# Performance work log

Hardware: AMD Instinct MI355X
Metric: run time of the kernel (lower is better)

Reference implementation:

```python
import jax, jax.numpy as jnp
import numpy as np

EPS = 1e-12

def setup_inputs() -> dict:
    key = jax.random.key(0)
    k1, k2, k3 = jax.random.split(key, 3)
    B, D, N, NCLS = 1024, 512, 100000, 1000
    z = jax.random.normal(k1, (B, D), dtype=jnp.float32)
    lab_bank = jax.random.normal(k2, (N, D), dtype=jnp.float32)
    lab_labels = jax.random.randint(k3, (N,), 0, NCLS, dtype=jnp.int64)
    return {"z": z, "lab_bank": lab_bank, "lab_labels": lab_labels, "topk": 5}

def reference(z, lab_bank, lab_labels, topk):
    # cosine similarity: normalize query and bank, then GEMM
    zn = z / jnp.maximum(jnp.linalg.norm(z, axis=-1, keepdims=True), EPS)            # [B, D]
    bn = lab_bank / jnp.maximum(jnp.linalg.norm(lab_bank, axis=-1, keepdims=True), EPS)  # [N, D]
    sim = jnp.einsum('bd,nd->bn', zn, bn)                                            # [B, N]
    top_vals, top_idx = jax.lax.top_k(sim, topk)                                     # [B, k] each
    labels = lab_labels[top_idx]                                                     # [B, k]
    return top_idx, top_vals, labels
```

## Files before the change

### kernel.cpp

```cpp
#include <hip/hip_runtime.h>
#include <math.h>

#define DDIM 512
#define NS 96
#define SPITCH 132
#define KMASK 0xFFFFF800
#define NEG_INF (-3.0e38f)
#define IMAX 0x7fffffff

typedef _Float16 f16x8 __attribute__((ext_vector_type(8)));
typedef float    f32x4 __attribute__((ext_vector_type(4)));
typedef int      i32x4 __attribute__((ext_vector_type(4)));

__device__ __forceinline__ int imin(int a, int b) { return a < b ? a : b; }
__device__ __forceinline__ int imax(int a, int b) { return a > b ? a : b; }

__device__ __forceinline__ int med3(int a, int b, int c) {
    int d;
    asm("v_med3_i32 %0, %1, %2, %3" : "=v"(d) : "v"(a), "v"(b), "v"(c));
    return d;
}

__device__ __forceinline__ void glds16(const void* g, void* l) {
    __builtin_amdgcn_global_load_lds((const __attribute__((address_space(1))) void*)g,
                                     (__attribute__((address_space(3))) void*)l, 16, 0, 0);
}

#define KBAR() do { asm volatile("s_waitcnt vmcnt(0)" ::: "memory"); \
                    __builtin_amdgcn_s_barrier();                    \
                    asm volatile("" ::: "memory"); } while (0)
#define EBAR() do { asm volatile("s_waitcnt lgkmcnt(0)" ::: "memory"); \
                    __builtin_amdgcn_s_barrier();                      \
                    asm volatile("" ::: "memory"); } while (0)

__global__ __launch_bounds__(256) void split_tile_k(const float* __restrict__ src,
                                                    unsigned* __restrict__ tile,
                                                    float* __restrict__ rn, int rows) {
    const int t = threadIdx.x;
    const int r = t >> 1, hf = t & 1;
    const int R = blockIdx.x * 128 + r;
    const bool valid = R < rows;
    const float* srow = src + (size_t)(valid ? R : 0) * DDIM + hf * 16;
    float ss = 0.f;
    for (int ks = 0; ks < 16; ++ks) {
        float4 v0 = *(const float4*)(srow + ks * 32);
        float4 v1 = *(const float4*)(srow + ks * 32 + 4);
        float4 v2 = *(const float4*)(srow + ks * 32 + 8);
        float4 v3 = *(const float4*)(srow + ks * 32 + 12);
        ss += v0.x*v0.x + v0.y*v0.y + v0.z*v0.z + v0.w*v0.w
            + v1.x*v1.x + v1.y*v1.y + v1.z*v1.z + v1.w*v1.w
            + v2.x*v2.x + v2.y*v2.y + v2.z*v2.z + v2.w*v2.w
            + v3.x*v3.x + v3.y*v3.y + v3.z*v3.z + v3.w*v3.w;
        unsigned o[8];
        o[0] = __builtin_bit_cast(unsigned, __builtin_amdgcn_cvt_pkrtz(v0.x, v0.y));
        o[1] = __builtin_bit_cast(unsigned, __builtin_amdgcn_cvt_pkrtz(v0.z, v0.w));
        o[2] = __builtin_bit_cast(unsigned, __builtin_amdgcn_cvt_pkrtz(v1.x, v1.y));
        o[3] = __builtin_bit_cast(unsigned, __builtin_amdgcn_cvt_pkrtz(v1.z, v1.w));
        o[4] = __builtin_bit_cast(unsigned, __builtin_amdgcn_cvt_pkrtz(v2.x, v2.y));
        o[5] = __builtin_bit_cast(unsigned, __builtin_amdgcn_cvt_pkrtz(v2.z, v2.w));
        o[6] = __builtin_bit_cast(unsigned, __builtin_amdgcn_cvt_pkrtz(v3.x, v3.y));
        o[7] = __builtin_bit_cast(unsigned, __builtin_amdgcn_cvt_pkrtz(v3.z, v3.w));
        if (!valid) {
            #pragma unroll
            for (int q = 0; q < 8; ++q) o[q] = 0u;
        }
        unsigned* dst = tile + ((size_t)(blockIdx.x * 16 + ks) * 128 + r) * 16 + hf * 8;
        *(i32x4*)dst       = *(i32x4*)o;
        *(i32x4*)(dst + 4) = *(i32x4*)(o + 4);
    }
    ss += __shfl_xor(ss, 1, 64);
    if (hf == 0) rn[R] = valid ? 1.0f / fmaxf(sqrtf(ss), 1e-12f) : 0.0f;
}

__global__ __launch_bounds__(256, 3) void gemm_screen_k(
    const unsigned* __restrict__ zh, const unsigned* __restrict__ bh,
    const float* __restrict__ rb,
    int* __restrict__ cand, int N, int nChunks) {

    __shared__ alignas(16) int smem[12544];
    int* SIMI = smem + 4096;

    const int t = threadIdx.x;
    const int w = t >> 6, lane = t & 63;
    const int wm = w & 1, wn = w >> 1;
    const int quad = lane >> 4, l16 = lane & 15;
    const int split = blockIdx.x, rowblk = blockIdx.y;
    const int soff = w * 1024 + lane * 16;

    int t0 = (int)0x80000000, t1 = t0, t2 = t0, t3 = t0;

    {
        const char* gA = (const char*)zh + (size_t)(rowblk * 16) * 8192;
        const char* gB = (const char*)bh + (size_t)(split * 16) * 8192;
        glds16(gA + soff,        (char*)smem + soff);
        glds16(gA + 4096 + soff, (char*)smem + 4096 + soff);
        glds16(gB + soff,        (char*)smem + 8192 + soff);
        glds16(gB + 4096 + soff, (char*)smem + 12288 + soff);
    }

    int iter = 0;
    for (int chunk = split; chunk < nChunks; chunk += NS, ++iter) {
        f32x4 acc[4][4];
        #pragma unroll
        for (int mi = 0; mi < 4; ++mi)
            #pragma unroll
            for (int ni = 0; ni < 4; ++ni) acc[mi][ni] = (f32x4){0.f, 0.f, 0.f, 0.f};
        float rbv[4];

        #pragma unroll 2
        for (int ks = 0; ks < 16; ++ks) {
            KBAR();
            if (ks < 15) {
                const char* gA = (const char*)zh + (size_t)(rowblk * 16 + ks + 1) * 8192;
                const char* gB = (const char*)bh + (size_t)(chunk * 16 + ks + 1) * 8192;
                char* l = (char*)smem + (((ks & 1) ^ 1) << 14);
                glds16(gA + soff,        l + soff);
                glds16(gA + 4096 + soff, l + 4096 + soff);
                glds16(gB + soff,        l + 8192 + soff);
                glds16(gB + 4096 + soff, l + 12288 + soff);
            } else if (chunk + NS < nChunks) {
                const char* gA = (const char*)zh + (size_t)(rowblk * 16) * 8192;
                const char* gB = (const char*)bh + (size_t)((chunk + NS) * 16) * 8192;
                glds16(gA + soff,        (char*)smem + soff);
                glds16(gA + 4096 + soff, (char*)smem + 4096 + soff);
                glds16(gB + soff,        (char*)smem + 8192 + soff);
                glds16(gB + 4096 + soff, (char*)smem + 12288 + soff);
            }
            if (ks == 0) {
                #pragma unroll
                for (int ni = 0; ni < 4; ++ni)
                    rbv[ni] = rb[chunk * 128 + wn * 64 + ni * 16 + l16];
            }

            const unsigned short* A  = (const unsigned short*)((const char*)smem + ((ks & 1) << 14));
            const unsigned short* Bb = (const unsigned short*)((const char*)smem + ((ks & 1) << 14) + 8192);
            f16x8 af[4], bf[4];
            #pragma unroll
            for (int mi = 0; mi < 4; ++mi)
                af[mi] = __builtin_bit_cast(f16x8,
                    *(const i32x4*)(A + (wm * 64 + mi * 16 + l16) * 32 + quad * 8));
            #pragma unroll
            for (int ni = 0; ni < 4; ++ni)
                bf[ni] = __builtin_bit_cast(f16x8,
                    *(const i32x4*)(Bb + (wn * 64 + ni * 16 + l16) * 32 + quad * 8));
            #pragma unroll
            for (int mi = 0; mi < 4; ++mi)
                #pragma unroll
                for (int ni = 0; ni < 4; ++ni)
                    acc[mi][ni] = __builtin_amdgcn_mfma_f32_16x16x32_f16(af[mi], bf[ni], acc[mi][ni], 0, 0, 0);
        }

        const int iterTag = iter << 7;
        #pragma unroll
        for (int p = 0; p < 2; ++p) {
            EBAR();
            #pragma unroll
            for (int nj = 0; nj < 2; ++nj) {
                const int ni = p * 2 + nj;
                const int cCol = wn * 64 + ni * 16 + l16;
                const int tagc = iterTag | cCol;
                const float rv = rbv[ni];
                const int cp = wn * 32 + nj * 16 + l16;
                #pragma unroll
                for (int mi = 0; mi < 4; ++mi) {
                    i32x4 kv;
                    #pragma unroll
                    for (int rr = 0; rr < 4; ++rr) {
                        float v = acc[mi][ni][rr] * rv;
                        kv[rr] = (__float_as_int(v) & KMASK) | tagc;
                    }
                    *(i32x4*)(SIMI + cp * SPITCH + wm * 64 + mi * 16 + quad * 4) = kv;
                }
            }
            EBAR();
            {
                const int r = t >> 1, h = t & 1;
                const int* s = SIMI + (h * 32) * SPITCH + r;
                #pragma unroll
                for (int j = 0; j < 32; ++j) {
                    int kk = s[j * SPITCH];
                    int n1 = med3(kk, t0, t1);
                    int n2 = med3(kk, t1, t2);
                    int n3 = med3(kk, t2, t3);
                    t0 = imax(kk, t0);
                    t1 = n1; t2 = n2; t3 = n3;
                }
            }
        }
    }

    const int r = t >> 1, h = t & 1;
    i32x4 outk = { t0, t1, t2, t3 };
    *(i32x4*)(cand + (((size_t)(rowblk * 128 + r) * NS + split) * 2 + h) * 4) = outk;
}

__global__ __launch_bounds__(256) void merge_rescore_k(
    const int* __restrict__ cand,
    const float* __restrict__ z, const float* __restrict__ bank,
    const float* __restrict__ rz, const float* __restrict__ rb,
    const int* __restrict__ labels, float* __restrict__ out, int BK, int N) {

    __shared__ float zrow[DDIM];
    __shared__ int   idxs[32];
    __shared__ float dots[32];

    const int row = blockIdx.x;
    const int t = threadIdx.x, w = t >> 6, lane = t & 63;

    {   float2 v = *(const float2*)(z + (size_t)row * DDIM + t * 2);
        zrow[t * 2] = v.x; zrow[t * 2 + 1] = v.y; }

    if (w == 0) {
        int k[12];
        const int* cp = cand + (size_t)row * (NS * 2 * 4) + lane * 12;
        #pragma unroll
        for (int q = 0; q < 12; ++q) k[q] = cp[q];
        for (int r = 0; r < 32; ++r) {
            int lk = k[0], lq = 0;
            #pragma unroll
            for (int q = 1; q < 12; ++q) if (k[q] > lk) { lk = k[q]; lq = q; }
            int wk = lk, wl = lane, wq = lq;
            #pragma unroll
            for (int off = 32; off > 0; off >>= 1) {
                int ok = __shfl_xor(wk, off, 64);
                int ol = __shfl_xor(wl, off, 64);
                int oq = __shfl_xor(wq, off, 64);
                if (ok > wk || (ok == wk && ol < wl)) { wk = ok; wl = ol; wq = oq; }
            }
            if (lane == wl) {
                #pragma unroll
                for (int q = 0; q < 12; ++q) if (q == wq) k[q] = (int)0x80000000;
            }
            if (lane == 0) {
                int j = wl * 12 + wq;
                int split = j >> 3;
                int c = wk & 127, it = (wk >> 7) & 15;
                int gi = (it * NS + split) * 128 + c;
                idxs[r] = gi < N ? gi : 0;
            }
        }
    }
    __syncthreads();

    #pragma unroll
    for (int jj = 0; jj < 8; ++jj) {
        const int ci = idxs[w * 8 + jj];
        const float* br = bank + (size_t)ci * DDIM + lane * 8;
        float4 x0 = *(const float4*)br;
        float4 x1 = *(const float4*)(br + 4);
        const float* zz = zrow + lane * 8;
        float4 z0 = *(const float4*)zz;
        float4 z1 = *(const float4*)(zz + 4);
        float s = x0.x*z0.x + x0.y*z0.y + x0.z*z0.z + x0.w*z0.w
                + x1.x*z1.x + x1.y*z1.y + x1.z*z1.z + x1.w*z1.w;
        #pragma unroll
        for (int off = 32; off > 0; off >>= 1) s += __shfl_xor(s, off, 64);
        if (lane == 0) dots[w * 8 + jj] = s;
    }
    __syncthreads();

    if (w == 0) {
        const float rzv = rz[row];
        float v; int ii;
        if (lane < 32) { ii = idxs[lane]; v = dots[lane] * rzv * rb[ii]; }
        else           { ii = IMAX;       v = NEG_INF; }
        for (int r = 0; r < 5; ++r) {
            float bv = v; int bi = ii;
            #pragma unroll
            for (int off = 32; off > 0; off >>= 1) {
                float ov = __shfl_xor(bv, off, 64);
                int   oi = __shfl_xor(bi, off, 64);
                if (ov > bv || (ov == bv && oi < bi)) { bv = ov; bi = oi; }
            }
            if (v == bv && ii == bi) { v = NEG_INF; ii = IMAX; }
            if (lane == 0) {
                out[(size_t)row * 5 + r]          = (float)bi;
                out[BK + (size_t)row * 5 + r]     = bv;
                out[2 * BK + (size_t)row * 5 + r] = (float)labels[bi];
            }
        }
    }
}

extern "C" void kernel_launch(void* const* d_in, const int* in_sizes, int n_in,
                              void* d_out, int out_size, void* d_ws, size_t ws_size,
                              hipStream_t stream) {
    const float* z    = (const float*)d_in[0];
    const float* bank = (const float*)d_in[1];
    const int*   lab  = (const int*)d_in[2];
    const int B = in_sizes[0] / DDIM;
    const int N = in_sizes[1] / DDIM;
    const int BK = out_size / 3;
    const int nChunks = (N + 127) >> 7;
    float* out = (float*)d_out;
    char* ws = (char*)d_ws;

    const size_t o_rz = 0;
    const size_t o_rb = 4096;
    const size_t o_zh = o_rb + (size_t)nChunks * 128 * 4;
    const size_t o_bh = o_zh + (size_t)(B / 128) * 16 * 8192;
    const size_t o_cv = o_bh + (size_t)nChunks * 16 * 8192;

    float* rz = (float*)(ws + o_rz);
    float* rb = (float*)(ws + o_rb);
    unsigned* zh = (unsigned*)(ws + o_zh);
    unsigned* bh = (unsigned*)(ws + o_bh);
    int* cand = (int*)(ws + o_cv);

    split_tile_k<<<nChunks, 256, 0, stream>>>(bank, bh, rb, N);
    split_tile_k<<<B / 128, 256, 0, stream>>>(z, zh, rz, B);
    gemm_screen_k<<<dim3(NS, B / 128), 256, 0, stream>>>(zh, bh, rb, cand, N, nChunks);
    merge_rescore_k<<<B, 256, 0, stream>>>(cand, z, bank, rz, rb, lab, out, BK, N);
}
```

Baseline: 484.1 us.

## Pre-normalize tiles and do top-4 screening in registers, dropping LDS transpose

The tiling kernel now computes the row norm first and writes already-normalized fp16 tiles, so the GEMM no longer loads or applies bank norms. The GEMM epilogue keeps per-thread top-4 lists in registers straight from the MFMA accumulators, with the operand order swapped so each lane holds consecutive bank columns. These lists are merged across lanes with shuffles at the end, which removes the shared-memory staging and its barriers and frees LDS for higher occupancy (launch bounds 3 -> 4). The two tiling launches are also merged into one. In exchange, the source rows are read twice in the tiling kernel and register pressure rises from 16 top-k slots per thread.

```diff
diff --git a/kernel.cpp b/kernel.cpp
--- a/kernel.cpp
+++ b/kernel.cpp
@@ -3,7 +3,6 @@
 
 #define DDIM 512
 #define NS 96
-#define SPITCH 132
 #define KMASK 0xFFFFF800
 #define NEG_INF (-3.0e38f)
 #define IMAX 0x7fffffff
@@ -29,18 +28,24 @@
 #define KBAR() do { asm volatile("s_waitcnt vmcnt(0)" ::: "memory"); \
                     __builtin_amdgcn_s_barrier();                    \
                     asm volatile("" ::: "memory"); } while (0)
-#define EBAR() do { asm volatile("s_waitcnt lgkmcnt(0)" ::: "memory"); \
-                    __builtin_amdgcn_s_barrier();                      \
-                    asm volatile("" ::: "memory"); } while (0)
-
-__global__ __launch_bounds__(256) void split_tile_k(const float* __restrict__ src,
-                                                    unsigned* __restrict__ tile,
-                                                    float* __restrict__ rn, int rows) {
+
+__global__ __launch_bounds__(256) void split_tile_k(
+    const float* __restrict__ zsrc, const float* __restrict__ bsrc,
+    unsigned* __restrict__ ztile, unsigned* __restrict__ btile,
+    float* __restrict__ rz, float* __restrict__ rb,
+    int zrows, int brows, int nbBlocks) {
+
+    const int bx = blockIdx.x;
+    const float* src; unsigned* tile; float* rn; int rows; int blk;
+    if (bx < nbBlocks) { src = bsrc; tile = btile; rn = rb; rows = brows; blk = bx; }
+    else               { src = zsrc; tile = ztile; rn = rz; rows = zrows; blk = bx - nbBlocks; }
+
     const int t = threadIdx.x;
     const int r = t >> 1, hf = t & 1;
-    const int R = blockIdx.x * 128 + r;
+    const int R = blk * 128 + r;
     const bool valid = R < rows;
     const float* srow = src + (size_t)(valid ? R : 0) * DDIM + hf * 16;
+
     float ss = 0.f;
     for (int ks = 0; ks < 16; ++ks) {
         float4 v0 = *(const float4*)(srow + ks * 32);
@@ -51,43 +56,49 @@
             + v1.x*v1.x + v1.y*v1.y + v1.z*v1.z + v1.w*v1.w
             + v2.x*v2.x + v2.y*v2.y + v2.z*v2.z + v2.w*v2.w
             + v3.x*v3.x + v3.y*v3.y + v3.z*v3.z + v3.w*v3.w;
+    }
+    ss += __shfl_xor(ss, 1, 64);
+    const float scale = valid ? 1.0f / fmaxf(sqrtf(ss), 1e-12f) : 0.0f;
+    if (hf == 0) rn[R] = scale;
+
+    for (int ks = 0; ks < 16; ++ks) {
+        float4 v0 = *(const float4*)(srow + ks * 32);
+        float4 v1 = *(const float4*)(srow + ks * 32 + 4);
+        float4 v2 = *(const float4*)(srow + ks * 32 + 8);
+        float4 v3 = *(const float4*)(srow + ks * 32 + 12);
         unsigned o[8];
-        o[0] = __builtin_bit_cast(unsigned, __builtin_amdgcn_cvt_pkrtz(v0.x, v0.y));
-        o[1] = __builtin_bit_cast(unsigned, __builtin_amdgcn_cvt_pkrtz(v0.z, v0.w));
-        o[2] = __builtin_bit_cast(unsigned, __builtin_amdgcn_cvt_pkrtz(v1.x, v1.y));
-        o[3] = __builtin_bit_cast(unsigned, __builtin_amdgcn_cvt_pkrtz(v1.z, v1.w));
-        o[4] = __builtin_bit_cast(unsigned, __builtin_amdgcn_cvt_pkrtz(v2.x, v2.y));
-        o[5] = __builtin_bit_cast(unsigned, __builtin_amdgcn_cvt_pkrtz(v2.z, v2.w));
-        o[6] = __builtin_bit_cast(unsigned, __builtin_amdgcn_cvt_pkrtz(v3.x, v3.y));
-        o[7] = __builtin_bit_cast(unsigned, __builtin_amdgcn_cvt_pkrtz(v3.z, v3.w));
-        if (!valid) {
-            #pragma unroll
-            for (int q = 0; q < 8; ++q) o[q] = 0u;
-        }
-        unsigned* dst = tile + ((size_t)(blockIdx.x * 16 + ks) * 128 + r) * 16 + hf * 8;
+        o[0] = __builtin_bit_cast(unsigned, __builtin_amdgcn_cvt_pkrtz(v0.x*scale, v0.y*scale));
+        o[1] = __builtin_bit_cast(unsigned, __builtin_amdgcn_cvt_pkrtz(v0.z*scale, v0.w*scale));
+        o[2] = __builtin_bit_cast(unsigned, __builtin_amdgcn_cvt_pkrtz(v1.x*scale, v1.y*scale));
+        o[3] = __builtin_bit_cast(unsigned, __builtin_amdgcn_cvt_pkrtz(v1.z*scale, v1.w*scale));
+        o[4] = __builtin_bit_cast(unsigned, __builtin_amdgcn_cvt_pkrtz(v2.x*scale, v2.y*scale));
+        o[5] = __builtin_bit_cast(unsigned, __builtin_amdgcn_cvt_pkrtz(v2.z*scale, v2.w*scale));
+        o[6] = __builtin_bit_cast(unsigned, __builtin_amdgcn_cvt_pkrtz(v3.x*scale, v3.y*scale));
+        o[7] = __builtin_bit_cast(unsigned, __builtin_amdgcn_cvt_pkrtz(v3.z*scale, v3.w*scale));
+        unsigned* dst = tile + ((size_t)(blk * 16 + ks) * 128 + r) * 16 + hf * 8;
         *(i32x4*)dst       = *(i32x4*)o;
         *(i32x4*)(dst + 4) = *(i32x4*)(o + 4);
     }
-    ss += __shfl_xor(ss, 1, 64);
-    if (hf == 0) rn[R] = valid ? 1.0f / fmaxf(sqrtf(ss), 1e-12f) : 0.0f;
-}
-
-__global__ __launch_bounds__(256, 3) void gemm_screen_k(
+}
+
+__global__ __launch_bounds__(256, 4) void gemm_screen_k(
     const unsigned* __restrict__ zh, const unsigned* __restrict__ bh,
-    const float* __restrict__ rb,
     int* __restrict__ cand, int N, int nChunks) {
 
-    __shared__ alignas(16) int smem[12544];
-    int* SIMI = smem + 4096;
+    __shared__ alignas(16) int smem[8192];
 
     const int t = threadIdx.x;
     const int w = t >> 6, lane = t & 63;
-    const int wm = w & 1, wn = w >> 1;
+    const int wz = w >> 1, wb = w & 1;
     const int quad = lane >> 4, l16 = lane & 15;
     const int split = blockIdx.x, rowblk = blockIdx.y;
     const int soff = w * 1024 + lane * 16;
 
-    int t0 = (int)0x80000000, t1 = t0, t2 = t0, t3 = t0;
+    int T[4][4];
+    #pragma unroll
+    for (int zi = 0; zi < 4; ++zi)
+        #pragma unroll
+        for (int q = 0; q < 4; ++q) T[zi][q] = (int)0x80000000;
 
     {
         const char* gA = (const char*)zh + (size_t)(rowblk * 16) * 8192;
@@ -102,10 +113,9 @@
     for (int chunk = split; chunk < nChunks; chunk += NS, ++iter) {
         f32x4 acc[4][4];
         #pragma unroll
-        for (int mi = 0; mi < 4; ++mi)
-            #pragma unroll
-            for (int ni = 0; ni < 4; ++ni) acc[mi][ni] = (f32x4){0.f, 0.f, 0.f, 0.f};
-        float rbv[4];
+        for (int bi = 0; bi < 4; ++bi)
+            #pragma unroll
+            for (int zi = 0; zi < 4; ++zi) acc[bi][zi] = (f32x4){0.f, 0.f, 0.f, 0.f};
 
         #pragma unroll 2
         for (int ks = 0; ks < 16; ++ks) {
@@ -126,72 +136,60 @@
                 glds16(gB + soff,        (char*)smem + 8192 + soff);
                 glds16(gB + 4096 + soff, (char*)smem + 12288 + soff);
             }
-            if (ks == 0) {
-                #pragma unroll
-                for (int ni = 0; ni < 4; ++ni)
-                    rbv[ni] = rb[chunk * 128 + wn * 64 + ni * 16 + l16];
-            }
 
             const unsigned short* A  = (const unsigned short*)((const char*)smem + ((ks & 1) << 14));
             const unsigned short* Bb = (const unsigned short*)((const char*)smem + ((ks & 1) << 14) + 8192);
             f16x8 af[4], bf[4];
             #pragma unroll
-            for (int mi = 0; mi < 4; ++mi)
-                af[mi] = __builtin_bit_cast(f16x8,
-                    *(const i32x4*)(A + (wm * 64 + mi * 16 + l16) * 32 + quad * 8));
-            #pragma unroll
-            for (int ni = 0; ni < 4; ++ni)
-                bf[ni] = __builtin_bit_cast(f16x8,
-                    *(const i32x4*)(Bb + (wn * 64 + ni * 16 + l16) * 32 + quad * 8));
-            #pragma unroll
-            for (int mi = 0; mi < 4; ++mi)
+            for (int zi = 0; zi < 4; ++zi)
+                af[zi] = __builtin_bit_cast(f16x8,
+                    *(const i32x4*)(A + (wz * 64 + zi * 16 + l16) * 32 + quad * 8));
+            #pragma unroll
+            for (int bi = 0; bi < 4; ++bi)
+                bf[bi] = __builtin_bit_cast(f16x8,
+                    *(const i32x4*)(Bb + (wb * 64 + bi * 16 + l16) * 32 + quad * 8));
+            #pragma unroll
+            for (int bi = 0; bi < 4; ++bi)
                 #pragma unroll
-                for (int ni = 0; ni < 4; ++ni)
-                    acc[mi][ni] = __builtin_amdgcn_mfma_f32_16x16x32_f16(af[mi], bf[ni], acc[mi][ni], 0, 0, 0);
-        }
-
-        const int iterTag = iter << 7;
-        #pragma unroll
-        for (int p = 0; p < 2; ++p) {
-            EBAR();
-            #pragma unroll
-            for (int nj = 0; nj < 2; ++nj) {
-                const int ni = p * 2 + nj;
-                const int cCol = wn * 64 + ni * 16 + l16;
-                const int tagc = iterTag | cCol;
-                const float rv = rbv[ni];
-                const int cp = wn * 32 + nj * 16 + l16;
+                for (int zi = 0; zi < 4; ++zi)
+                    acc[bi][zi] = __builtin_amdgcn_mfma_f32_16x16x32_f16(bf[bi], af[zi], acc[bi][zi], 0, 0, 0);
+        }
+
+        const int tbase = (iter << 7) | (wb << 6) | (quad << 2);
+        #pragma unroll
+        for (int zi = 0; zi < 4; ++zi)
+            #pragma unroll
+            for (int bi = 0; bi < 4; ++bi)
                 #pragma unroll
-                for (int mi = 0; mi < 4; ++mi) {
-                    i32x4 kv;
-                    #pragma unroll
-                    for (int rr = 0; rr < 4; ++rr) {
-                        float v = acc[mi][ni][rr] * rv;
-                        kv[rr] = (__float_as_int(v) & KMASK) | tagc;
-                    }
-                    *(i32x4*)(SIMI + cp * SPITCH + wm * 64 + mi * 16 + quad * 4) = kv;
+                for (int rr = 0; rr < 4; ++rr) {
+                    int kk = (__float_as_int(acc[bi][zi][rr]) & KMASK) | (tbase + bi * 16 + rr);
+                    int n1 = med3(kk, T[zi][0], T[zi][1]);
+                    int n2 = med3(kk, T[zi][1], T[zi][2]);
+                    int n3 = med3(kk, T[zi][2], T[zi][3]);
+                    T[zi][0] = imax(kk, T[zi][0]);
+                    T[zi][1] = n1; T[zi][2] = n2; T[zi][3] = n3;
                 }
-            }
-            EBAR();
-            {
-                const int r = t >> 1, h = t & 1;
-                const int* s = SIMI + (h * 32) * SPITCH + r;
-                #pragma unroll
-                for (int j = 0; j < 32; ++j) {
-                    int kk = s[j * SPITCH];
-                    int n1 = med3(kk, t0, t1);
-                    int n2 = med3(kk, t1, t2);
-                    int n3 = med3(kk, t2, t3);
-                    t0 = imax(kk, t0);
-                    t1 = n1; t2 = n2; t3 = n3;
-                }
-            }
-        }
-    }
-
-    const int r = t >> 1, h = t & 1;
-    i32x4 outk = { t0, t1, t2, t3 };
-    *(i32x4*)(cand + (((size_t)(rowblk * 128 + r) * NS + split) * 2 + h) * 4) = outk;
+    }
+
+    #pragma unroll
+    for (int zi = 0; zi < 4; ++zi) {
+        int a0 = T[zi][0], a1 = T[zi][1], a2 = T[zi][2], a3 = T[zi][3];
+        #pragma unroll
+        for (int off = 16; off <= 32; off <<= 1) {
+            int p0 = __shfl_xor(a0, off, 64);
+            int p1 = __shfl_xor(a1, off, 64);
+            int p2 = __shfl_xor(a2, off, 64);
+            int p3 = __shfl_xor(a3, off, 64);
+            int m0 = imax(a0, p3), m1 = imax(a1, p2), m2 = imax(a2, p1), m3 = imax(a3, p0);
+            int b0 = imax(m0, m2), b2 = imin(m0, m2), b1 = imax(m1, m3), b3 = imin(m1, m3);
+            a0 = imax(b0, b1); a1 = imin(b0, b1); a2 = imax(b2, b3); a3 = imin(b2, b3);
+        }
+        if (quad == 0) {
+            i32x4 outk = { a0, a1, a2, a3 };
+            const int row = rowblk * 128 + wz * 64 + zi * 16 + l16;
+            *(i32x4*)(cand + (((size_t)row * NS + split) * 2 + wb) * 4) = outk;
+        }
+    }
 }
 
 __global__ __launch_bounds__(256) void merge_rescore_k(
@@ -307,8 +305,7 @@
     unsigned* bh = (unsigned*)(ws + o_bh);
     int* cand = (int*)(ws + o_cv);
 
-    split_tile_k<<<nChunks, 256, 0, stream>>>(bank, bh, rb, N);
-    split_tile_k<<<B / 128, 256, 0, stream>>>(z, zh, rz, B);
-    gemm_screen_k<<<dim3(NS, B / 128), 256, 0, stream>>>(zh, bh, rb, cand, N, nChunks);
+    split_tile_k<<<nChunks + B / 128, 256, 0, stream>>>(z, bank, zh, bh, rz, rb, B, N, nChunks);
+    gemm_screen_k<<<dim3(NS, B / 128), 256, 0, stream>>>(zh, bh, cand, N, nChunks);
     merge_rescore_k<<<B, 256, 0, stream>>>(cand, z, bank, rz, rb, lab, out, BK, N);
 }
```

New measurement: 489.8 us. No clear change (+1.2%).
